# Kernel tuning notes

Hardware: AMD Instinct MI355X
Metric: run time of the kernel (lower is better)

The kernel has to match this reference:

```python
import jax, jax.numpy as jnp
import numpy as np

N_NODES = 100000
N_EDGES = 1600000
IN_FEATS = 128
OUT_FEATS = 128


def setup_inputs() -> dict:
    key = jax.random.key(0)
    k1, k2, k3, k4, k5 = jax.random.split(key, 5)
    feature = jax.random.normal(k1, (N_NODES, IN_FEATS), dtype=jnp.float32)
    src = jax.random.randint(k2, (N_EDGES,), 0, N_NODES, dtype=jnp.int64)
    dst = jax.random.randint(k3, (N_EDGES,), 0, N_NODES, dtype=jnp.int64)
    # nn.Linear default init: U(-1/sqrt(in), 1/sqrt(in)); randn scaled is fine for a numeric baseline
    bound = 1.0 / np.sqrt(IN_FEATS)
    W = jax.random.uniform(k4, (OUT_FEATS, IN_FEATS), dtype=jnp.float32, minval=-bound, maxval=bound)
    b = jax.random.uniform(k5, (OUT_FEATS,), dtype=jnp.float32, minval=-bound, maxval=bound)
    return {"feature": feature, "src": src, "dst": dst, "W": W, "b": b}


def reference(feature, src, dst, W, b):
    # message passing: copy source feature along each edge, sum into destination node
    agg = jax.ops.segment_sum(feature[src], dst, num_segments=N_NODES)  # [N, in_feats]
    # node apply: ReLU(Linear(h))
    return jax.nn.relu(agg @ W.T + b)  # [N, out_feats]
```

## Files before the change

### kernel.cpp

```cpp
#include <hip/hip_runtime.h>

#define N_NODES 100000
#define N_EDGES 1600000
#define F 128

#define NB    1563
#define NBP2  2048
#define CAP   1280
#define CHUNK 8192

#define BIN_BLOCKS  196
#define FEAT_BLOCKS 3125
#define WCONV_BLOCKS 16
#define FRONT_GRID  (BIN_BLOCKS + FEAT_BLOCKS + WCONV_BLOCKS)

#define LDP  136

typedef __bf16  bf16x8 __attribute__((ext_vector_type(8)));
typedef float   f32x4  __attribute__((ext_vector_type(4)));

__device__ inline unsigned short f32_to_bf16(float f) {
    unsigned u = __builtin_bit_cast(unsigned, f);
    u += 0x7FFFu + ((u >> 16) & 1u);
    return (unsigned short)(u >> 16);
}
__device__ inline unsigned pack_bf16x2(float lo, float hi) {
    return (unsigned)f32_to_bf16(lo) | ((unsigned)f32_to_bf16(hi) << 16);
}
__device__ inline void addrow(float* acc, const uint4 v) {
    acc[0] += __builtin_bit_cast(float, v.x << 16);
    acc[1] += __builtin_bit_cast(float, v.x & 0xFFFF0000u);
    acc[2] += __builtin_bit_cast(float, v.y << 16);
    acc[3] += __builtin_bit_cast(float, v.y & 0xFFFF0000u);
    acc[4] += __builtin_bit_cast(float, v.z << 16);
    acc[5] += __builtin_bit_cast(float, v.z & 0xFFFF0000u);
    acc[6] += __builtin_bit_cast(float, v.w << 16);
    acc[7] += __builtin_bit_cast(float, v.w & 0xFFFF0000u);
}

__global__ __launch_bounds__(1024) void gcn_front(
    const float* __restrict__ feat, const float* __restrict__ W,
    const int* __restrict__ src, const int* __restrict__ dst,
    int* __restrict__ gcur, unsigned* __restrict__ bins,
    unsigned short* __restrict__ Wbf,
    char* __restrict__ featdst, int fstride)
{
    __shared__ unsigned cnt[NBP2];
    __shared__ unsigned off[NBP2];
    __shared__ int      gbase[NBP2];
    __shared__ unsigned staged[CHUNK];
    __shared__ unsigned short sbk[CHUNK];
    __shared__ unsigned scan[1024];

    const int tid = threadIdx.x;
    const int bx  = blockIdx.x;

    if (bx >= BIN_BLOCKS) {
        const int rb = bx - BIN_BLOCKS;
        if (rb < FEAT_BLOCKS) {
            const int t = rb * 1024 + tid;
            const float4 v = *(const float4*)(feat + (size_t)t * 4);
            uint2 p;
            p.x = pack_bf16x2(v.x, v.y);
            p.y = pack_bf16x2(v.z, v.w);
            const int n = t >> 5, q = t & 31;
            *(uint2*)(featdst + (size_t)n * fstride + q * 8) = p;
        } else {
            const int i = (rb - FEAT_BLOCKS) * 1024 + tid;
            Wbf[i] = f32_to_bf16(W[i]);
        }
        return;
    }

    const int e0 = bx * CHUNK;

    #pragma unroll
    for (int i = 0; i < 2; ++i) cnt[tid + i * 1024] = 0;
    __syncthreads();

    int sv[8], dv[8];
    #pragma unroll
    for (int i = 0; i < 8; ++i) {
        const int e = e0 + tid + i * 1024;
        if (e < N_EDGES) {
            sv[i] = src[e];
            dv[i] = dst[e];
            atomicAdd(&cnt[dv[i] >> 6], 1u);
        } else dv[i] = -1;
    }
    __syncthreads();

    const unsigned s = cnt[2 * tid] + cnt[2 * tid + 1];
    scan[tid] = s;
    __syncthreads();
    for (int o = 1; o < 1024; o <<= 1) {
        const unsigned t = (tid >= o) ? scan[tid - o] : 0;
        __syncthreads();
        scan[tid] += t;
        __syncthreads();
    }
    const unsigned run = scan[tid] - s;
    off[2 * tid]     = run;
    off[2 * tid + 1] = run + cnt[2 * tid];
    __syncthreads();

    #pragma unroll
    for (int i = 0; i < 8; ++i) {
        if (dv[i] >= 0) {
            const int bk = dv[i] >> 6;
            const unsigned w = (unsigned)sv[i] | ((unsigned)(dv[i] & 63) << 17);
            const unsigned p = atomicAdd(&off[bk], 1u);
            staged[p] = w;
            sbk[p] = (unsigned short)bk;
        }
    }
    __syncthreads();

    #pragma unroll
    for (int i = 0; i < 2; ++i) {
        const int bk = 2 * tid + i;
        if (bk < NB && cnt[bk] > 0)
            gbase[bk] = atomicAdd(&gcur[bk], (int)cnt[bk]);
    }
    __syncthreads();

    const int c_tot = (int)scan[1023];
    for (int p = tid; p < c_tot; p += 1024) {
        const int bk = sbk[p];
        const int gp = gbase[bk] + (p - (int)(off[bk] - cnt[bk]));
        if (gp < CAP) bins[(size_t)bk * CAP + gp] = staged[p];
    }
}

__global__ __launch_bounds__(512) void gcn_accum_gemm(
    const int* __restrict__ gcur,
    const unsigned* __restrict__ bins,
    const unsigned short* __restrict__ featbf,
    const unsigned short* __restrict__ Wbf,
    const float* __restrict__ b,
    float* __restrict__ out)
{
    __shared__ unsigned tmp[CAP];
    __shared__ unsigned list[CAP];
    __shared__ int cnt64[64], scn[64], pos64[64], cur64[64];
    __shared__ unsigned short Alds[64 * LDP];
    __shared__ unsigned short Wlds[F * LDP];

    const int tid = threadIdx.x;
    const int bkt = blockIdx.x;

    #pragma unroll
    for (int i = 0; i < 4; ++i) {
        const int c2 = tid + i * 512;
        const int r = c2 >> 4, cc = c2 & 15;
        *(uint4*)&Wlds[r * LDP + cc * 8] = *(const uint4*)&Wbf[c2 * 8];
    }

    int c = gcur[bkt]; if (c > CAP) c = CAP;
    const unsigned* bb = bins + (size_t)bkt * CAP;

    for (int i = tid; i < c; i += 512) tmp[i] = bb[i];
    if (tid < 64) cnt64[tid] = 0;
    __syncthreads();

    for (int i = tid; i < c; i += 512) atomicAdd(&cnt64[(tmp[i] >> 17) & 63], 1);
    __syncthreads();

    if (tid < 64) scn[tid] = cnt64[tid];
    __syncthreads();
    #pragma unroll
    for (int o = 1; o < 64; o <<= 1) {
        int t = 0;
        if (tid < 64 && tid >= o) t = scn[tid - o];
        __syncthreads();
        if (tid < 64) scn[tid] += t;
        __syncthreads();
    }
    if (tid < 64) {
        const int st = scn[tid] - cnt64[tid];
        pos64[tid] = st;
        cur64[tid] = st;
    }
    __syncthreads();

    for (int i = tid; i < c; i += 512) {
        const unsigned w = tmp[i];
        const int p = atomicAdd(&cur64[(w >> 17) & 63], 1);
        list[p] = w;
    }
    __syncthreads();

    const int grp = tid >> 4;
    const int sl  = tid & 15;
    const int n0  = bkt * 64;

    #pragma unroll
    for (int ni = 0; ni < 2; ++ni) {
        const int l  = grp * 2 + ni;
        const int st = pos64[l];
        const int en = st + cnt64[l];

        float a0[8] = {0,0,0,0,0,0,0,0};
        float a1[8] = {0,0,0,0,0,0,0,0};
        int k = st;
        for (; k + 3 < en; k += 4) {
            const unsigned w0 = list[k],     w1 = list[k + 1];
            const unsigned w2 = list[k + 2], w3 = list[k + 3];
            const uint4 v0 = *(const uint4*)((const char*)featbf + (size_t)(w0 & 0x1FFFF) * 256 + sl * 16);
            const uint4 v1 = *(const uint4*)((const char*)featbf + (size_t)(w1 & 0x1FFFF) * 256 + sl * 16);
            const uint4 v2 = *(const uint4*)((const char*)featbf + (size_t)(w2 & 0x1FFFF) * 256 + sl * 16);
            const uint4 v3 = *(const uint4*)((const char*)featbf + (size_t)(w3 & 0x1FFFF) * 256 + sl * 16);
            addrow(a0, v0); addrow(a1, v1); addrow(a0, v2); addrow(a1, v3);
        }
        for (; k < en; ++k) {
            const unsigned w0 = list[k];
            const uint4 v0 = *(const uint4*)((const char*)featbf + (size_t)(w0 & 0x1FFFF) * 256 + sl * 16);
            addrow(a0, v0);
        }
        #pragma unroll
        for (int q = 0; q < 8; ++q) a0[q] += a1[q];

        uint4 o;
        o.x = pack_bf16x2(a0[0], a0[1]);
        o.y = pack_bf16x2(a0[2], a0[3]);
        o.z = pack_bf16x2(a0[4], a0[5]);
        o.w = pack_bf16x2(a0[6], a0[7]);
        *(uint4*)&Alds[l * LDP + sl * 8] = o;
    }
    __syncthreads();

    const int lane = tid & 63;
    const int wv   = tid >> 6;
    const int lr   = lane & 15;
    const int lq   = lane >> 4;
    const int rf   = wv >> 1;
    const int ch   = (wv & 1) * 4;

    f32x4 acc[4] = {};
    #pragma unroll
    for (int kk = 0; kk < 4; ++kk) {
        const bf16x8 a = __builtin_bit_cast(bf16x8,
            *(const uint4*)&Alds[(rf * 16 + lr) * LDP + kk * 32 + lq * 8]);
        bf16x8 w[4];
        #pragma unroll
        for (int n = 0; n < 4; ++n)
            w[n] = __builtin_bit_cast(bf16x8,
                *(const uint4*)&Wlds[((ch + n) * 16 + lr) * LDP + kk * 32 + lq * 8]);
        #pragma unroll
        for (int n = 0; n < 4; ++n)
            acc[n] = __builtin_amdgcn_mfma_f32_16x16x32_bf16(a, w[n], acc[n], 0, 0, 0);
    }

    float bs[4];
    #pragma unroll
    for (int n = 0; n < 4; ++n) bs[n] = b[(ch + n) * 16 + lr];

    #pragma unroll
    for (int rg = 0; rg < 4; ++rg) {
        const int row = rf * 16 + lq * 4 + rg;
        const int gn  = n0 + row;
        if (gn < N_NODES) {
            float* orow = out + (size_t)gn * F;
            #pragma unroll
            for (int n = 0; n < 4; ++n) {
                const float v = acc[n][rg] + bs[n];
                orow[(ch + n) * 16 + lr] = v > 0.0f ? v : 0.0f;
            }
        }
    }
}

__global__ __launch_bounds__(512) void gcn_accum2(
    const int* __restrict__ gcur,
    const unsigned* __restrict__ bins,
    float* __restrict__ out)
{
    __shared__ unsigned tmp[CAP];
    __shared__ unsigned list[CAP];
    __shared__ int cnt64[64], scn[64], pos64[64], cur64[64];

    const int tid = threadIdx.x;
    const int bkt = blockIdx.x;

    int c = gcur[bkt]; if (c > CAP) c = CAP;
    const unsigned* bb = bins + (size_t)bkt * CAP;

    for (int i = tid; i < c; i += 512) tmp[i] = bb[i];
    if (tid < 64) cnt64[tid] = 0;
    __syncthreads();
    for (int i = tid; i < c; i += 512) atomicAdd(&cnt64[(tmp[i] >> 17) & 63], 1);
    __syncthreads();
    if (tid < 64) scn[tid] = cnt64[tid];
    __syncthreads();
    #pragma unroll
    for (int o = 1; o < 64; o <<= 1) {
        int t = 0;
        if (tid < 64 && tid >= o) t = scn[tid - o];
        __syncthreads();
        if (tid < 64) scn[tid] += t;
        __syncthreads();
    }
    if (tid < 64) {
        const int st = scn[tid] - cnt64[tid];
        pos64[tid] = st;
        cur64[tid] = st;
    }
    __syncthreads();
    for (int i = tid; i < c; i += 512) {
        const unsigned w = tmp[i];
        const int p = atomicAdd(&cur64[(w >> 17) & 63], 1);
        list[p] = w;
    }
    __syncthreads();

    const int grp = tid >> 4, sl = tid & 15, n0 = bkt * 64;
    #pragma unroll
    for (int ni = 0; ni < 2; ++ni) {
        const int l  = grp * 2 + ni;
        const int st = pos64[l];
        const int en = st + cnt64[l];
        float a0[8] = {0,0,0,0,0,0,0,0};
        float a1[8] = {0,0,0,0,0,0,0,0};
        int k = st;
        for (; k + 3 < en; k += 4) {
            const unsigned w0 = list[k],     w1 = list[k + 1];
            const unsigned w2 = list[k + 2], w3 = list[k + 3];
            const uint4 v0 = *(const uint4*)((const char*)out + (size_t)(w0 & 0x1FFFF) * 512 + sl * 16);
            const uint4 v1 = *(const uint4*)((const char*)out + (size_t)(w1 & 0x1FFFF) * 512 + sl * 16);
            const uint4 v2 = *(const uint4*)((const char*)out + (size_t)(w2 & 0x1FFFF) * 512 + sl * 16);
            const uint4 v3 = *(const uint4*)((const char*)out + (size_t)(w3 & 0x1FFFF) * 512 + sl * 16);
            addrow(a0, v0); addrow(a1, v1); addrow(a0, v2); addrow(a1, v3);
        }
        for (; k < en; ++k) {
            const unsigned w0 = list[k];
            const uint4 v0 = *(const uint4*)((const char*)out + (size_t)(w0 & 0x1FFFF) * 512 + sl * 16);
            addrow(a0, v0);
        }
        #pragma unroll
        for (int q = 0; q < 8; ++q) a0[q] += a1[q];
        const int n = n0 + l;
        if (n < N_NODES) {
            uint4 o;
            o.x = pack_bf16x2(a0[0], a0[1]);
            o.y = pack_bf16x2(a0[2], a0[3]);
            o.z = pack_bf16x2(a0[4], a0[5]);
            o.w = pack_bf16x2(a0[6], a0[7]);
            *(uint4*)((char*)out + (size_t)n * 512 + 256 + sl * 16) = o;
        }
    }
}

#define MT 128
__global__ __launch_bounds__(256) void gcn_gemm_mfma(
    float* __restrict__ out,
    const unsigned short* __restrict__ Wbf,
    const float* __restrict__ b)
{
    __shared__ unsigned short Alds[MT * LDP];
    __shared__ unsigned short Wlds[F * LDP];

    const int tid  = threadIdx.x;
    const int row0 = blockIdx.x * MT;

    #pragma unroll
    for (int i = 0; i < 8; ++i) {
        const int c = tid + i * 256;
        const int r = c >> 4, cc = c & 15;
        *(uint4*)&Wlds[r * LDP + cc * 8] = *(const uint4*)&Wbf[c * 8];
    }
    #pragma unroll
    for (int i = 0; i < 8; ++i) {
        const int c = tid + i * 256;
        const int r = c >> 4, cc = c & 15;
        int gr = row0 + r; if (gr > N_NODES - 1) gr = N_NODES - 1;
        const uint4 v = *(const uint4*)((const char*)out + (size_t)gr * 512 + 256 + cc * 16);
        *(uint4*)&Alds[r * LDP + cc * 8] = v;
    }
    __syncthreads();

    const int lane = tid & 63;
    const int wv   = tid >> 6;
    const int lr   = lane & 15;
    const int lq   = lane >> 4;

    f32x4 acc[2][8] = {};
    #pragma unroll
    for (int kk = 0; kk < 4; ++kk) {
        bf16x8 a[2], w[8];
        #pragma unroll
        for (int i = 0; i < 2; ++i)
            a[i] = __builtin_bit_cast(bf16x8,
                *(const uint4*)&Alds[(wv * 32 + i * 16 + lr) * LDP + kk * 32 + lq * 8]);
        #pragma unroll
        for (int n = 0; n < 8; ++n)
            w[n] = __builtin_bit_cast(bf16x8,
                *(const uint4*)&Wlds[(n * 16 + lr) * LDP + kk * 32 + lq * 8]);
        #pragma unroll
        for (int i = 0; i < 2; ++i)
            #pragma unroll
            for (int n = 0; n < 8; ++n)
                acc[i][n] = __builtin_amdgcn_mfma_f32_16x16x32_bf16(a[i], w[n], acc[i][n], 0, 0, 0);
    }

    float bias[8];
    #pragma unroll
    for (int n = 0; n < 8; ++n) bias[n] = b[n * 16 + lr];

    #pragma unroll
    for (int i = 0; i < 2; ++i) {
        const int rbase = wv * 32 + i * 16 + lq * 4;
        #pragma unroll
        for (int rg = 0; rg < 4; ++rg) {
            const int gr = row0 + rbase + rg;
            if (gr < N_NODES) {
                float* orow = out + (size_t)gr * F;
                #pragma unroll
                for (int n = 0; n < 8; ++n) {
                    const float v = acc[i][n][rg] + bias[n];
                    orow[n * 16 + lr] = v > 0.0f ? v : 0.0f;
                }
            }
        }
    }
}

__global__ __launch_bounds__(256) void gcn_scatter(
    const float* __restrict__ feat,
    const int* __restrict__ src, const int* __restrict__ dst,
    float* __restrict__ agg)
{
    const int sub  = threadIdx.x >> 5;
    const int lane = threadIdx.x & 31;
    const long long e = (long long)blockIdx.x * 8 + sub;
    if (e >= N_EDGES) return;
    const int s = src[e], d = dst[e];
    const float4 v = *(const float4*)(feat + (size_t)s * F + lane * 4);
    float* ar = agg + (size_t)d * F + lane * 4;
    unsafeAtomicAdd(ar + 0, v.x);
    unsafeAtomicAdd(ar + 1, v.y);
    unsafeAtomicAdd(ar + 2, v.z);
    unsafeAtomicAdd(ar + 3, v.w);
}

#define GR  64
#define LDW 132
__global__ __launch_bounds__(256) void gcn_gemm_relu(
    float* __restrict__ agg_out,
    const float* __restrict__ W, const float* __restrict__ b)
{
    __shared__ float Wl[F][LDW];
    __shared__ float At[GR][LDW];
    const int tid = threadIdx.x;
    const long long row0 = (long long)blockIdx.x * GR;
    #pragma unroll
    for (int i = 0; i < 64; ++i) {
        const int e = tid + i * 256;
        Wl[e >> 7][e & 127] = W[e];
    }
    #pragma unroll
    for (int i = 0; i < 32; ++i) {
        const int e = tid + i * 256;
        const int r = e >> 7, k2 = e & 127;
        const long long gr = row0 + r;
        At[r][k2] = (gr < N_NODES) ? agg_out[gr * F + k2] : 0.0f;
    }
    __syncthreads();
    const int tx = tid & 15, ty = tid >> 4, r0 = ty * 4;
    float acc[4][8];
    #pragma unroll
    for (int r = 0; r < 4; ++r)
        #pragma unroll
        for (int m = 0; m < 8; ++m) acc[r][m] = 0.0f;
    for (int k0 = 0; k0 < F; k0 += 4) {
        float4 a[4], w[8];
        #pragma unroll
        for (int r = 0; r < 4; ++r) a[r] = *(const float4*)&At[r0 + r][k0];
        #pragma unroll
        for (int m = 0; m < 8; ++m) w[m] = *(const float4*)&Wl[tx + 16 * m][k0];
        #pragma unroll
        for (int r = 0; r < 4; ++r)
            #pragma unroll
            for (int m = 0; m < 8; ++m)
                acc[r][m] += a[r].x * w[m].x + a[r].y * w[m].y
                           + a[r].z * w[m].z + a[r].w * w[m].w;
    }
    float bias[8];
    #pragma unroll
    for (int m = 0; m < 8; ++m) bias[m] = b[tx + 16 * m];
    __syncthreads();
    #pragma unroll
    for (int r = 0; r < 4; ++r) {
        const long long gr = row0 + r0 + r;
        if (gr < N_NODES) {
            float* orow = agg_out + gr * F;
            #pragma unroll
            for (int m = 0; m < 8; ++m) {
                const float v = acc[r][m] + bias[m];
                orow[tx + 16 * m] = v > 0.0f ? v : 0.0f;
            }
        }
    }
}

extern "C" void kernel_launch(void* const* d_in, const int* in_sizes, int n_in,
                              void* d_out, int out_size, void* d_ws, size_t ws_size,
                              hipStream_t stream) {
    const float* feat = (const float*)d_in[0];
    const int*   src  = (const int*)d_in[1];
    const int*   dst  = (const int*)d_in[2];
    const float* W    = (const float*)d_in[3];
    const float* b    = (const float*)d_in[4];
    float* out = (float*)d_out;

    const size_t ws_base = 1600u * 4 + (size_t)NB * CAP * 4 + (size_t)F * F * 2;
    const size_t ws_full = ws_base + (size_t)N_NODES * F * 2;

    if (ws_size >= ws_base) {
        int* gcur = (int*)d_ws;
        unsigned* bins = (unsigned*)(gcur + 1600);
        unsigned short* Wbf = (unsigned short*)(bins + (size_t)NB * CAP);
        unsigned short* featbf = Wbf + (size_t)F * F;

        hipMemsetAsync(gcur, 0, NB * sizeof(int), stream);

        if (ws_size >= ws_full) {
            gcn_front<<<FRONT_GRID, 1024, 0, stream>>>(
                feat, W, src, dst, gcur, bins, Wbf, (char*)featbf, 256);
            gcn_accum_gemm<<<NB, 512, 0, stream>>>(gcur, bins, featbf, Wbf, b, out);
        } else {
            gcn_front<<<FRONT_GRID, 1024, 0, stream>>>(
                feat, W, src, dst, gcur, bins, Wbf, (char*)out, 512);
            gcn_accum2<<<NB, 512, 0, stream>>>(gcur, bins, out);
            gcn_gemm_mfma<<<(N_NODES + MT - 1) / MT, 256, 0, stream>>>(out, Wbf, b);
        }
    } else {
        hipMemsetAsync(out, 0, (size_t)N_NODES * F * sizeof(float), stream);
        gcn_scatter<<<N_EDGES / 8, 256, 0, stream>>>(feat, src, dst, out);
        gcn_gemm_relu<<<(N_NODES + GR - 1) / GR, 256, 0, stream>>>(out, W, b);
    }
}
```

Baseline: 196.0 us.

## Split fused accumulate-GEMM into sort, feature-sliced gather, and separate MFMA GEMM

```diff
diff --git a/kernel.cpp b/kernel.cpp
--- a/kernel.cpp
+++ b/kernel.cpp
@@ -7,6 +7,7 @@
 #define NB    1563
 #define NBP2  2048
 #define CAP   1280
+#define CMAX  1215
 #define CHUNK 8192
 
 #define BIN_BLOCKS  196
@@ -64,7 +65,13 @@
             p.x = pack_bf16x2(v.x, v.y);
             p.y = pack_bf16x2(v.z, v.w);
             const int n = t >> 5, q = t & 31;
-            *(uint2*)(featdst + (size_t)n * fstride + q * 8) = p;
+            if (fstride == 0) {
+                const int fs = q >> 2, j2 = q & 3;
+                *(uint2*)(featdst + (size_t)fs * ((size_t)N_NODES * 32)
+                                  + (size_t)n * 32 + j2 * 8) = p;
+            } else {
+                *(uint2*)(featdst + (size_t)n * fstride + q * 8) = p;
+            }
         } else {
             const int i = (rb - FEAT_BLOCKS) * 1024 + tid;
             Wbf[i] = f32_to_bf16(W[i]);
@@ -128,42 +135,28 @@
     for (int p = tid; p < c_tot; p += 1024) {
         const int bk = sbk[p];
         const int gp = gbase[bk] + (p - (int)(off[bk] - cnt[bk]));
-        if (gp < CAP) bins[(size_t)bk * CAP + gp] = staged[p];
-    }
-}
-
-__global__ __launch_bounds__(512) void gcn_accum_gemm(
-    const int* __restrict__ gcur,
-    const unsigned* __restrict__ bins,
-    const unsigned short* __restrict__ featbf,
-    const unsigned short* __restrict__ Wbf,
-    const float* __restrict__ b,
-    float* __restrict__ out)
-{
-    __shared__ unsigned tmp[CAP];
-    __shared__ unsigned list[CAP];
+        if (gp < CMAX) bins[(size_t)bk * CAP + gp] = staged[p];
+    }
+}
+
+__global__ __launch_bounds__(256) void gcn_sort(
+    const int* __restrict__ gcur, unsigned* __restrict__ bins)
+{
+    __shared__ unsigned tmp[CMAX];
+    __shared__ unsigned list[CMAX];
     __shared__ int cnt64[64], scn[64], pos64[64], cur64[64];
-    __shared__ unsigned short Alds[64 * LDP];
-    __shared__ unsigned short Wlds[F * LDP];
 
     const int tid = threadIdx.x;
     const int bkt = blockIdx.x;
 
-    #pragma unroll
-    for (int i = 0; i < 4; ++i) {
-        const int c2 = tid + i * 512;
-        const int r = c2 >> 4, cc = c2 & 15;
-        *(uint4*)&Wlds[r * LDP + cc * 8] = *(const uint4*)&Wbf[c2 * 8];
-    }
-
-    int c = gcur[bkt]; if (c > CAP) c = CAP;
-    const unsigned* bb = bins + (size_t)bkt * CAP;
-
-    for (int i = tid; i < c; i += 512) tmp[i] = bb[i];
+    int c = gcur[bkt]; if (c > CMAX) c = CMAX;
+    unsigned* bb = bins + (size_t)bkt * CAP;
+
+    for (int i = tid; i < c; i += 256) tmp[i] = bb[i];
     if (tid < 64) cnt64[tid] = 0;
     __syncthreads();
 
-    for (int i = tid; i < c; i += 512) atomicAdd(&cnt64[(tmp[i] >> 17) & 63], 1);
+    for (int i = tid; i < c; i += 256) atomicAdd(&cnt64[(tmp[i] >> 17) & 63], 1);
     __syncthreads();
 
     if (tid < 64) scn[tid] = cnt64[tid];
@@ -183,49 +176,95 @@
     }
     __syncthreads();
 
-    for (int i = tid; i < c; i += 512) {
+    for (int i = tid; i < c; i += 256) {
         const unsigned w = tmp[i];
-        const int p = atomicAdd(&cur64[(w >> 17) & 63], 1);
-        list[p] = w;
-    }
-    __syncthreads();
-
-    const int grp = tid >> 4;
-    const int sl  = tid & 15;
-    const int n0  = bkt * 64;
-
-    #pragma unroll
-    for (int ni = 0; ni < 2; ++ni) {
-        const int l  = grp * 2 + ni;
-        const int st = pos64[l];
-        const int en = st + cnt64[l];
-
-        float a0[8] = {0,0,0,0,0,0,0,0};
-        float a1[8] = {0,0,0,0,0,0,0,0};
-        int k = st;
-        for (; k + 3 < en; k += 4) {
-            const unsigned w0 = list[k],     w1 = list[k + 1];
-            const unsigned w2 = list[k + 2], w3 = list[k + 3];
-            const uint4 v0 = *(const uint4*)((const char*)featbf + (size_t)(w0 & 0x1FFFF) * 256 + sl * 16);
-            const uint4 v1 = *(const uint4*)((const char*)featbf + (size_t)(w1 & 0x1FFFF) * 256 + sl * 16);
-            const uint4 v2 = *(const uint4*)((const char*)featbf + (size_t)(w2 & 0x1FFFF) * 256 + sl * 16);
-            const uint4 v3 = *(const uint4*)((const char*)featbf + (size_t)(w3 & 0x1FFFF) * 256 + sl * 16);
-            addrow(a0, v0); addrow(a1, v1); addrow(a0, v2); addrow(a1, v3);
-        }
-        for (; k < en; ++k) {
-            const unsigned w0 = list[k];
-            const uint4 v0 = *(const uint4*)((const char*)featbf + (size_t)(w0 & 0x1FFFF) * 256 + sl * 16);
-            addrow(a0, v0);
-        }
-        #pragma unroll
-        for (int q = 0; q < 8; ++q) a0[q] += a1[q];
-
+        list[atomicAdd(&cur64[(w >> 17) & 63], 1)] = w;
+    }
+    __syncthreads();
+
+    for (int i = tid; i < c; i += 256) bb[i] = list[i];
+    if (tid < 64) bb[CMAX + tid] = (unsigned)pos64[tid];
+    if (tid == 64) bb[CAP - 1] = (unsigned)c;
+}
+
+__global__ __launch_bounds__(256) void gcn_gatherx(
+    const int* __restrict__ gcur,
+    const unsigned* __restrict__ bins,
+    const unsigned short* __restrict__ featbf,
+    float* __restrict__ out)
+{
+    const int bx   = blockIdx.x;
+    const int fs   = bx & 7;
+    const int pair = bx >> 3;
+    const int tid  = threadIdx.x;
+    const int bkt  = pair * 2 + (tid >> 7);
+    if (bkt >= NB) return;
+    const int l = (tid >> 1) & 63;
+    const int j = tid & 1;
+
+    const unsigned* bb = bins + (size_t)bkt * CAP;
+    const int st = (int)bb[CMAX + l];
+    int en;
+    if (l == 63) { en = gcur[bkt]; if (en > CMAX) en = CMAX; }
+    else         { en = (int)bb[CMAX + l + 1]; }
+
+    const char* base = (const char*)featbf + (size_t)fs * ((size_t)N_NODES * 32) + j * 16;
+
+    float a0[8] = {0,0,0,0,0,0,0,0};
+    float a1[8] = {0,0,0,0,0,0,0,0};
+    int k = st;
+    for (; k + 3 < en; k += 4) {
+        const unsigned w0 = bb[k],     w1 = bb[k + 1];
+        const unsigned w2 = bb[k + 2], w3 = bb[k + 3];
+        const uint4 v0 = *(const uint4*)(base + (size_t)(w0 & 0x1FFFF) * 32);
+        const uint4 v1 = *(const uint4*)(base + (size_t)(w1 & 0x1FFFF) * 32);
+        const uint4 v2 = *(const uint4*)(base + (size_t)(w2 & 0x1FFFF) * 32);
+        const uint4 v3 = *(const uint4*)(base + (size_t)(w3 & 0x1FFFF) * 32);
+        addrow(a0, v0); addrow(a1, v1); addrow(a0, v2); addrow(a1, v3);
+    }
+    for (; k < en; ++k) {
+        const uint4 v0 = *(const uint4*)(base + (size_t)(bb[k] & 0x1FFFF) * 32);
+        addrow(a0, v0);
+    }
+    #pragma unroll
+    for (int q = 0; q < 8; ++q) a0[q] += a1[q];
+
+    const int n = bkt * 64 + l;
+    if (n < N_NODES) {
         uint4 o;
         o.x = pack_bf16x2(a0[0], a0[1]);
         o.y = pack_bf16x2(a0[2], a0[3]);
         o.z = pack_bf16x2(a0[4], a0[5]);
         o.w = pack_bf16x2(a0[6], a0[7]);
-        *(uint4*)&Alds[l * LDP + sl * 8] = o;
+        *(uint4*)((char*)out + (size_t)n * 512 + 256 + fs * 32 + j * 16) = o;
+    }
+}
+
+#define MT 128
+__global__ __launch_bounds__(256) void gcn_gemm_mfma(
+    float* __restrict__ out,
+    const unsigned short* __restrict__ Wbf,
+    const float* __restrict__ b)
+{
+    __shared__ unsigned short Alds[MT * LDP];
+    __shared__ unsigned short Wlds[F * LDP];
+
+    const int tid  = threadIdx.x;
+    const int row0 = blockIdx.x * MT;
+
+    #pragma unroll
+    for (int i = 0; i < 8; ++i) {
+        const int c = tid + i * 256;
+        const int r = c >> 4, cc = c & 15;
+        *(uint4*)&Wlds[r * LDP + cc * 8] = *(const uint4*)&Wbf[c * 8];
+    }
+    #pragma unroll
+    for (int i = 0; i < 8; ++i) {
+        const int c = tid + i * 256;
+        const int r = c >> 4, cc = c & 15;
+        int gr = row0 + r; if (gr > N_NODES - 1) gr = N_NODES - 1;
+        const uint4 v = *(const uint4*)((const char*)out + (size_t)gr * 512 + 256 + cc * 16);
+        *(uint4*)&Alds[r * LDP + cc * 8] = v;
     }
     __syncthreads();
 
@@ -233,38 +272,43 @@
     const int wv   = tid >> 6;
     const int lr   = lane & 15;
     const int lq   = lane >> 4;
-    const int rf   = wv >> 1;
-    const int ch   = (wv & 1) * 4;
-
-    f32x4 acc[4] = {};
+
+    f32x4 acc[2][8] = {};
     #pragma unroll
     for (int kk = 0; kk < 4; ++kk) {
-        const bf16x8 a = __builtin_bit_cast(bf16x8,
-            *(const uint4*)&Alds[(rf * 16 + lr) * LDP + kk * 32 + lq * 8]);
-        bf16x8 w[4];
-        #pragma unroll
-        for (int n = 0; n < 4; ++n)
+        bf16x8 a[2], w[8];
+        #pragma unroll
+        for (int i = 0; i < 2; ++i)
+            a[i] = __builtin_bit_cast(bf16x8,
+                *(const uint4*)&Alds[(wv * 32 + i * 16 + lr) * LDP + kk * 32 + lq * 8]);
+        #pragma unroll
+        for (int n = 0; n < 8; ++n)
             w[n] = __builtin_bit_cast(bf16x8,
-                *(const uint4*)&Wlds[((ch + n) * 16 + lr) * LDP + kk * 32 + lq * 8]);
-        #pragma unroll
-        for (int n = 0; n < 4; ++n)
-            acc[n] = __builtin_amdgcn_mfma_f32_16x16x32_bf16(a, w[n], acc[n], 0, 0, 0);
-    }
-
-    float bs[4];
-    #pragma unroll
-    for (int n = 0; n < 4; ++n) bs[n] = b[(ch + n) * 16 + lr];
-
-    #pragma unroll
-    for (int rg = 0; rg < 4; ++rg) {
-        const int row = rf * 16 + lq * 4 + rg;
-        const int gn  = n0 + row;
-        if (gn < N_NODES) {
-            float* orow = out + (size_t)gn * F;
+                *(const uint4*)&Wlds[(n * 16 + lr) * LDP + kk * 32 + lq * 8]);
+        #pragma unroll
+        for (int i = 0; i < 2; ++i)
             #pragma unroll
-            for (int n = 0; n < 4; ++n) {
-                const float v = acc[n][rg] + bs[n];
-                orow[(ch + n) * 16 + lr] = v > 0.0f ? v : 0.0f;
+            for (int n = 0; n < 8; ++n)
+                acc[i][n] = __builtin_amdgcn_mfma_f32_16x16x32_bf16(a[i], w[n], acc[i][n], 0, 0, 0);
+    }
+
+    float bias[8];
+    #pragma unroll
+    for (int n = 0; n < 8; ++n) bias[n] = b[n * 16 + lr];
+
+    #pragma unroll
+    for (int i = 0; i < 2; ++i) {
+        const int rbase = wv * 32 + i * 16 + lq * 4;
+        #pragma unroll
+        for (int rg = 0; rg < 4; ++rg) {
+            const int gr = row0 + rbase + rg;
+            if (gr < N_NODES) {
+                float* orow = out + (size_t)gr * F;
+                #pragma unroll
+                for (int n = 0; n < 8; ++n) {
+                    const float v = acc[i][n][rg] + bias[n];
+                    orow[n * 16 + lr] = v > 0.0f ? v : 0.0f;
+                }
             }
         }
     }
@@ -275,14 +319,14 @@
     const unsigned* __restrict__ bins,
     float* __restrict__ out)
 {
-    __shared__ unsigned tmp[CAP];
-    __shared__ unsigned list[CAP];
+    __shared__ unsigned tmp[CMAX];
+    __shared__ unsigned list[CMAX];
     __shared__ int cnt64[64], scn[64], pos64[64], cur64[64];
 
     const int tid = threadIdx.x;
     const int bkt = blockIdx.x;
 
-    int c = gcur[bkt]; if (c > CAP) c = CAP;
+    int c = gcur[bkt]; if (c > CMAX) c = CMAX;
     const unsigned* bb = bins + (size_t)bkt * CAP;
 
     for (int i = tid; i < c; i += 512) tmp[i] = bb[i];
@@ -308,8 +352,7 @@
     __syncthreads();
     for (int i = tid; i < c; i += 512) {
         const unsigned w = tmp[i];
-        const int p = atomicAdd(&cur64[(w >> 17) & 63], 1);
-        list[p] = w;
+        list[atomicAdd(&cur64[(w >> 17) & 63], 1)] = w;
     }
     __syncthreads();
 
@@ -332,8 +375,7 @@
             addrow(a0, v0); addrow(a1, v1); addrow(a0, v2); addrow(a1, v3);
         }
         for (; k < en; ++k) {
-            const unsigned w0 = list[k];
-            const uint4 v0 = *(const uint4*)((const char*)out + (size_t)(w0 & 0x1FFFF) * 512 + sl * 16);
+            const uint4 v0 = *(const uint4*)((const char*)out + (size_t)(list[k] & 0x1FFFF) * 512 + sl * 16);
             addrow(a0, v0);
         }
         #pragma unroll
@@ -346,80 +388,6 @@
             o.z = pack_bf16x2(a0[4], a0[5]);
             o.w = pack_bf16x2(a0[6], a0[7]);
             *(uint4*)((char*)out + (size_t)n * 512 + 256 + sl * 16) = o;
-        }
-    }
-}
-
-#define MT 128
-__global__ __launch_bounds__(256) void gcn_gemm_mfma(
-    float* __restrict__ out,
-    const unsigned short* __restrict__ Wbf,
-    const float* __restrict__ b)
-{
-    __shared__ unsigned short Alds[MT * LDP];
-    __shared__ unsigned short Wlds[F * LDP];
-
-    const int tid  = threadIdx.x;
-    const int row0 = blockIdx.x * MT;
-
-    #pragma unroll
-    for (int i = 0; i < 8; ++i) {
-        const int c = tid + i * 256;
-        const int r = c >> 4, cc = c & 15;
-        *(uint4*)&Wlds[r * LDP + cc * 8] = *(const uint4*)&Wbf[c * 8];
-    }
-    #pragma unroll
-    for (int i = 0; i < 8; ++i) {
-        const int c = tid + i * 256;
-        const int r = c >> 4, cc = c & 15;
-        int gr = row0 + r; if (gr > N_NODES - 1) gr = N_NODES - 1;
-        const uint4 v = *(const uint4*)((const char*)out + (size_t)gr * 512 + 256 + cc * 16);
-        *(uint4*)&Alds[r * LDP + cc * 8] = v;
-    }
-    __syncthreads();
-
-    const int lane = tid & 63;
-    const int wv   = tid >> 6;
-    const int lr   = lane & 15;
-    const int lq   = lane >> 4;
-
-    f32x4 acc[2][8] = {};
-    #pragma unroll
-    for (int kk = 0; kk < 4; ++kk) {
-        bf16x8 a[2], w[8];
-        #pragma unroll
-        for (int i = 0; i < 2; ++i)
-            a[i] = __builtin_bit_cast(bf16x8,
-                *(const uint4*)&Alds[(wv * 32 + i * 16 + lr) * LDP + kk * 32 + lq * 8]);
-        #pragma unroll
-        for (int n = 0; n < 8; ++n)
-            w[n] = __builtin_bit_cast(bf16x8,
-                *(const uint4*)&Wlds[(n * 16 + lr) * LDP + kk * 32 + lq * 8]);
-        #pragma unroll
-        for (int i = 0; i < 2; ++i)
-            #pragma unroll
-            for (int n = 0; n < 8; ++n)
-                acc[i][n] = __builtin_amdgcn_mfma_f32_16x16x32_bf16(a[i], w[n], acc[i][n], 0, 0, 0);
-    }
-
-    float bias[8];
-    #pragma unroll
-    for (int n = 0; n < 8; ++n) bias[n] = b[n * 16 + lr];
-
-    #pragma unroll
-    for (int i = 0; i < 2; ++i) {
-        const int rbase = wv * 32 + i * 16 + lq * 4;
-        #pragma unroll
-        for (int rg = 0; rg < 4; ++rg) {
-            const int gr = row0 + rbase + rg;
-            if (gr < N_NODES) {
-                float* orow = out + (size_t)gr * F;
-                #pragma unroll
-                for (int n = 0; n < 8; ++n) {
-                    const float v = acc[i][n][rg] + bias[n];
-                    orow[n * 16 + lr] = v > 0.0f ? v : 0.0f;
-                }
-            }
         }
     }
 }
@@ -525,8 +493,11 @@
 
         if (ws_size >= ws_full) {
             gcn_front<<<FRONT_GRID, 1024, 0, stream>>>(
-                feat, W, src, dst, gcur, bins, Wbf, (char*)featbf, 256);
-            gcn_accum_gemm<<<NB, 512, 0, stream>>>(gcur, bins, featbf, Wbf, b, out);
+                feat, W, src, dst, gcur, bins, Wbf, (char*)featbf, 0);
+            gcn_sort<<<NB, 256, 0, stream>>>(gcur, bins);
+            const int pairs = (NB + 1) / 2;
+            gcn_gatherx<<<pairs * 8, 256, 0, stream>>>(gcur, bins, featbf, out);
+            gcn_gemm_mfma<<<(N_NODES + MT - 1) / MT, 256, 0, stream>>>(out, Wbf, b);
         } else {
             gcn_front<<<FRONT_GRID, 1024, 0, stream>>>(
                 feat, W, src, dst, gcur, bins, Wbf, (char*)out, 512);
```

New measurement: 238.7 us. 1.22x slower.
